# Kernel optimization log

Hardware: AMD Instinct MI355X
Metric: run time of the kernel (lower is better)

Reference implementation:

```python
import jax, jax.numpy as jnp
import numpy as np

LORA_SCALING = 1.0 / 4.0  # lora_alpha / lora_rank
NUM_HEADS = 16
HEAD_DIM = 64
ROPE_BASE = 20000.0


def rotate_half(x):
    x1, x2 = jnp.split(x, 2, axis=-1)
    return jnp.concatenate([-x2, x1], axis=-1)


def setup_inputs() -> dict:
    key = jax.random.key(0)
    ks = jax.random.split(key, 8)
    B, S, D = 8, 1024, 1024
    hidden_states = jax.random.normal(ks[0], (B, S, D), jnp.float32)
    attention_mask = jnp.zeros((B, 1, 1, S), jnp.float32)
    # real rotary tables (HF style: duplicated half-dim freqs)
    inv_freq = 1.0 / (ROPE_BASE ** (jnp.arange(0, HEAD_DIM, 2, dtype=jnp.float32) / HEAD_DIM))
    t = jnp.arange(S, dtype=jnp.float32)
    freqs = jnp.outer(t, inv_freq)                      # [S, hd/2]
    emb = jnp.concatenate([freqs, freqs], axis=-1)      # [S, hd]
    cos = jnp.broadcast_to(jnp.cos(emb)[None], (B, S, HEAD_DIM))
    sin = jnp.broadcast_to(jnp.sin(emb)[None], (B, S, HEAD_DIM))
    adapter_mask = jax.random.randint(ks[1], (B,), 0, 5, jnp.int32)
    Wqkv_weight = jax.random.normal(ks[2], (3 * D, D), jnp.float32) * 0.02
    Wqkv_bias = jax.random.normal(ks[3], (3 * D,), jnp.float32) * 0.02
    lora_A = jax.random.normal(ks[4], (5, 4, D), jnp.float32) * 0.02
    lora_B = jax.random.normal(ks[5], (5, 3 * D, 4), jnp.float32) * 0.02
    return dict(hidden_states=hidden_states, attention_mask=attention_mask,
                cos=cos, sin=sin, adapter_mask=adapter_mask,
                Wqkv_weight=Wqkv_weight, Wqkv_bias=Wqkv_bias,
                lora_A=lora_A, lora_B=lora_B)


def reference(hidden_states, attention_mask, cos, sin, adapter_mask,
              Wqkv_weight, Wqkv_bias, lora_A, lora_B):
    B, S, D = hidden_states.shape
    H, hd = NUM_HEADS, HEAD_DIM
    # fused QKV projection with per-task LoRA (gather adapters per batch row)
    base = jnp.einsum('bsd,od->bso', hidden_states, Wqkv_weight) + Wqkv_bias
    A_t = lora_A[adapter_mask]                    # [B, r, D]
    B_t = lora_B[adapter_mask]                    # [B, 3D, r]
    lo = jnp.einsum('bsd,brd->bsr', hidden_states, A_t)
    delta = jnp.einsum('bsr,bor->bso', lo, B_t) * LORA_SCALING
    qkv = (base + delta).reshape(B, S, 3, H, hd)
    q = qkv[:, :, 0].transpose(0, 2, 1, 3)        # [B,H,S,hd]
    k = qkv[:, :, 1].transpose(0, 2, 1, 3)
    v = qkv[:, :, 2].transpose(0, 2, 1, 3)
    # inline RoPE
    c = cos[:, None, :, :]
    s = sin[:, None, :, :]
    q = q * c + rotate_half(q) * s
    k = k * c + rotate_half(k) * s
    # eager SDPA
    scaling = hd ** -0.5
    scores = jnp.einsum('bhqd,bhkd->bhqk', q, k) * scaling + attention_mask
    attn = jax.nn.softmax(scores, axis=-1)
    out = jnp.einsum('bhqk,bhkd->bhqd', attn, v)
    return out.transpose(0, 2, 1, 3).reshape(B, S, H * hd)
```

## Files before the change

### kernel.cpp

```cpp
#include <hip/hip_runtime.h>
#include <hip/hip_bf16.h>
#include <stdint.h>

typedef __attribute__((ext_vector_type(8))) short short8;
typedef __attribute__((ext_vector_type(4))) float f32x4;
typedef unsigned short ushort_t;

#define MFMA16(a, b, c) __builtin_amdgcn_mfma_f32_16x16x32_bf16((a), (b), (c), 0, 0, 0)
#define EXP2F(x) __builtin_amdgcn_exp2f(x)
#define BAR() __builtin_amdgcn_s_barrier()


__device__ __forceinline__ float bf2f(unsigned short u) {
    union { unsigned int i; float f; } x; x.i = ((unsigned int)u) << 16; return x.f;
}
__device__ __forceinline__ unsigned short f2bf(float f) {
    union { float f; unsigned int i; } x; x.f = f;
    unsigned int i = x.i;
    i = i + 0x7FFFu + ((i >> 16) & 1u);
    return (unsigned short)(i >> 16);
}
__device__ __forceinline__ unsigned int pack2(float a, float b) {
    return (unsigned int)f2bf(a) | ((unsigned int)f2bf(b) << 16);
}
__device__ __forceinline__ void glds16(const void* gsrc, void* ldst) {
    __builtin_amdgcn_global_load_lds(
        (const __attribute__((address_space(1))) unsigned int*)gsrc,
        (__attribute__((address_space(3))) unsigned int*)ldst, 16, 0, 0);
}

__global__ __launch_bounds__(256) void prep_kernel(
    const float* __restrict__ hidden,
    const float* __restrict__ W,
    const float* __restrict__ loraA,
    const int* __restrict__ adapter_mask,
    ushort_t* __restrict__ Hb,
    ushort_t* __restrict__ Wb,
    float4* __restrict__ lo)
{
    int tid = threadIdx.x;
    int wave = tid >> 6, lane = tid & 63;
    int row = blockIdx.x * 4 + wave;
    if (row < 8192) {
        int b = row >> 10;
        int a = adapter_mask[b];
        const float4* hp = (const float4*)(hidden + (size_t)row * 1024);
        float4 hv[4];
#pragma unroll
        for (int c = 0; c < 4; ++c) hv[c] = hp[c * 64 + lane];
#pragma unroll
        for (int c = 0; c < 4; ++c) {
            uint2 pk;
            pk.x = pack2(hv[c].x, hv[c].y);
            pk.y = pack2(hv[c].z, hv[c].w);
            *(uint2*)(Hb + (size_t)row * 1024 + c * 256 + lane * 4) = pk;
        }
        const float4* Ap = (const float4*)(loraA + (size_t)a * 4096);
        float acc[4];
#pragma unroll
        for (int r = 0; r < 4; ++r) {
            float s = 0.f;
#pragma unroll
            for (int c = 0; c < 4; ++c) {
                float4 av = Ap[(size_t)r * 256 + c * 64 + lane];
                s += hv[c].x * av.x + hv[c].y * av.y + hv[c].z * av.z + hv[c].w * av.w;
            }
            acc[r] = s;
        }
        for (int off = 32; off > 0; off >>= 1)
#pragma unroll
            for (int r = 0; r < 4; ++r) acc[r] += __shfl_xor(acc[r], off);
        if (lane == 0) lo[row] = make_float4(acc[0], acc[1], acc[2], acc[3]);
    } else {
        int rw = row - 8192;
        const float4* wp = (const float4*)(W + (size_t)rw * 1024);
        float4 wv[4];
#pragma unroll
        for (int c = 0; c < 4; ++c) wv[c] = wp[c * 64 + lane];
#pragma unroll
        for (int c = 0; c < 4; ++c) {
            uint2 pk;
            pk.x = pack2(wv[c].x, wv[c].y);
            pk.y = pack2(wv[c].z, wv[c].w);
            *(uint2*)(Wb + (size_t)rw * 1024 + c * 256 + lane * 4) = pk;
        }
    }
}

__global__ __launch_bounds__(512, 2) void qkv_gemm_kernel(
    const ushort_t* __restrict__ Hb,
    const ushort_t* __restrict__ Wb,
    const float* __restrict__ bias,
    const float4* __restrict__ lo,
    const float* __restrict__ loraB,
    const int* __restrict__ adapter_mask,
    const float* __restrict__ cosp,
    const float* __restrict__ sinp,
    ushort_t* __restrict__ qw,
    ushort_t* __restrict__ kw,
    ushort_t* __restrict__ vt)
{
    __shared__ __align__(16) ushort_t As[2][16384];
    __shared__ __align__(16) ushort_t Bs[2][16384];
    int tid = threadIdx.x;
    int wave = tid >> 6, lane = tid & 63, quad = lane >> 4, l16 = lane & 15;
    int wm = wave >> 2, wn = wave & 3;

    int wg = (blockIdx.x & 7) * 48 + (blockIdx.x >> 3);
    int bx = wg % 12, by = wg / 12;
    int n0 = bx * 256;
    int m0 = by * 256;

    int r_ = tid >> 3, c_ = (tid & 7) ^ (r_ & 7);
    const ushort_t* pA0 = Hb + (size_t)(m0 +   0 + r_) * 1024 + c_ * 8;
    const ushort_t* pA1 = Hb + (size_t)(m0 +  64 + r_) * 1024 + c_ * 8;
    const ushort_t* pA2 = Hb + (size_t)(m0 + 128 + r_) * 1024 + c_ * 8;
    const ushort_t* pA3 = Hb + (size_t)(m0 + 192 + r_) * 1024 + c_ * 8;
    const ushort_t* pB0 = Wb + (size_t)(n0 +   0 + r_) * 1024 + c_ * 8;
    const ushort_t* pB1 = Wb + (size_t)(n0 +  64 + r_) * 1024 + c_ * 8;
    const ushort_t* pB2 = Wb + (size_t)(n0 + 128 + r_) * 1024 + c_ * 8;
    const ushort_t* pB3 = Wb + (size_t)(n0 + 192 + r_) * 1024 + c_ * 8;
    char* stA0 = (char*)&As[0][0] + wave * 1024;
    char* stB0 = (char*)&Bs[0][0] + wave * 1024;

    f32x4 acc[8][4];
#pragma unroll
    for (int i = 0; i < 8; ++i)
#pragma unroll
        for (int j = 0; j < 4; ++j) acc[i][j] = (f32x4)0.f;

    glds16(pB0, stB0);          glds16(pB1, stB0 + 8192);
    glds16(pB2, stB0 + 16384);  glds16(pB3, stB0 + 24576);
    glds16(pA0, stA0);          glds16(pA1, stA0 + 8192);
    glds16(pA2, stA0 + 16384);  glds16(pA3, stA0 + 24576);
    glds16(pB0 + 64, stB0 + 32768);          glds16(pB1 + 64, stB0 + 32768 + 8192);
    glds16(pB2 + 64, stB0 + 32768 + 16384);  glds16(pB3 + 64, stB0 + 32768 + 24576);

#pragma unroll 2
    for (int t = 0; t < 16; ++t) {
        int cur = t & 1;
        const char* rdA = (const char*)&As[0][0] + cur * 32768;
        const char* rdB = (const char*)&Bs[0][0] + cur * 32768;
        char* sA = stA0 + (cur ^ 1) * 32768;
        char* sB = stB0 + cur * 32768;
        int kA = (t + 1) << 6;
        int kB = (t + 2) << 6;

        if (t < 15) { asm volatile("s_waitcnt vmcnt(4)" ::: "memory"); }
        else        { asm volatile("s_waitcnt vmcnt(0)" ::: "memory"); }
        BAR();
        if (t < 15) {
            glds16(pA0 + kA, sA);          glds16(pA1 + kA, sA + 8192);
            glds16(pA2 + kA, sA + 16384);  glds16(pA3 + kA, sA + 24576);
        }
        short8 bfr[4][2];
#pragma unroll
        for (int ni = 0; ni < 4; ++ni) {
            int rb = ni * 16 + l16;
            bfr[ni][0] = *(const short8*)(rdB + wn * 8192 + (rb * 8 + ((quad    ) ^ (rb & 7))) * 16);
            bfr[ni][1] = *(const short8*)(rdB + wn * 8192 + (rb * 8 + ((quad + 4) ^ (rb & 7))) * 16);
        }
        asm volatile("s_waitcnt lgkmcnt(0)" ::: "memory");
        BAR();
        if (t < 14) {
            glds16(pB0 + kB, sB);          glds16(pB1 + kB, sB + 8192);
            glds16(pB2 + kB, sB + 16384);  glds16(pB3 + kB, sB + 24576);
        }
        __builtin_amdgcn_s_setprio(1);
#pragma unroll
        for (int mi = 0; mi < 8; ++mi) {
            int u = wm * 2 + (mi >> 2);
            int rr = (mi & 3) * 16 + l16;
            short8 a0 = *(const short8*)(rdA + u * 8192 + (rr * 8 + ((quad    ) ^ (rr & 7))) * 16);
            short8 a1 = *(const short8*)(rdA + u * 8192 + (rr * 8 + ((quad + 4) ^ (rr & 7))) * 16);
            acc[mi][0] = MFMA16(a0, bfr[0][0], acc[mi][0]);
            acc[mi][1] = MFMA16(a0, bfr[1][0], acc[mi][1]);
            acc[mi][2] = MFMA16(a0, bfr[2][0], acc[mi][2]);
            acc[mi][3] = MFMA16(a0, bfr[3][0], acc[mi][3]);
            acc[mi][0] = MFMA16(a1, bfr[0][1], acc[mi][0]);
            acc[mi][1] = MFMA16(a1, bfr[1][1], acc[mi][1]);
            acc[mi][2] = MFMA16(a1, bfr[2][1], acc[mi][2]);
            acc[mi][3] = MFMA16(a1, bfr[3][1], acc[mi][3]);
        }
        __builtin_amdgcn_s_setprio(0);
    }

    int t_qkv = n0 >> 10;
    int b = m0 >> 10;
    int a_idx = adapter_mask[b];
    float bi[4], bb[4][4];
    int cpos[4], chh[4];
#pragma unroll
    for (int ni = 0; ni < 4; ++ni) {
        int c = n0 + wn * 64 + ni * 16 + l16;
        bi[ni] = bias[c];
        const float* Bp = loraB + ((size_t)a_idx * 3072 + c) * 4;
        bb[ni][0] = Bp[0]; bb[ni][1] = Bp[1]; bb[ni][2] = Bp[2]; bb[ni][3] = Bp[3];
        cpos[ni] = c & 63; chh[ni] = (c >> 6) & 15;
    }
#pragma unroll
    for (int mi = 0; mi < 8; ++mi) {
        float vals[4][4];
        int mrow0 = m0 + wm * 128 + mi * 16 + quad * 4;
#pragma unroll
        for (int r = 0; r < 4; ++r) {
            float4 lov = lo[mrow0 + r];
#pragma unroll
            for (int ni = 0; ni < 4; ++ni)
                vals[r][ni] = acc[mi][ni][r] + bi[ni]
                      + 0.25f * (lov.x * bb[ni][0] + lov.y * bb[ni][1]
                               + lov.z * bb[ni][2] + lov.w * bb[ni][3]);
        }
        int s0 = mrow0 & 1023;
        if (t_qkv < 2) {
#pragma unroll
            for (int r = 0; r < 4; ++r) {
                int s = s0 + r;
                size_t cb = ((size_t)b * 1024 + s) * 64;
                float cA = cosp[cb + l16],      sA_ = sinp[cb + l16];
                float cB = cosp[cb + 16 + l16], sB_ = sinp[cb + 16 + l16];
                float w0 = vals[r][0] * cA - vals[r][2] * sA_;
                float w2 = vals[r][2] * cA + vals[r][0] * sA_;
                float w1 = vals[r][1] * cB - vals[r][3] * sB_;
                float w3 = vals[r][3] * cB + vals[r][1] * sB_;
                float v[4] = {w0, w1, w2, w3};
#pragma unroll
                for (int ni = 0; ni < 4; ++ni) {
                    size_t bh = (size_t)b * 16 + chh[ni];
                    ushort_t ob = f2bf(v[ni]);
                    if (t_qkv == 0) qw[(bh * 1024 + s) * 64 + cpos[ni]] = ob;
                    else            kw[(bh * 1024 + s) * 64 + cpos[ni]] = ob;
                }
            }
        } else {
#pragma unroll
            for (int ni = 0; ni < 4; ++ni) {
                uint2 pk;
                pk.x = pack2(vals[0][ni], vals[1][ni]);
                pk.y = pack2(vals[2][ni], vals[3][ni]);
                size_t bh = (size_t)b * 16 + chh[ni];
                *(uint2*)&vt[(bh * 64 + cpos[ni]) * 1024 + s0] = pk;
            }
        }
    }
}

__global__ __launch_bounds__(256, 2) void attn_kernel(
    const ushort_t* __restrict__ qw,
    const ushort_t* __restrict__ kw,
    const ushort_t* __restrict__ vt,
    const float* __restrict__ mask,
    float* __restrict__ out)
{
    __shared__ __align__(16) ushort_t Kt[3][4096];
    __shared__ __align__(16) ushort_t Vt[3][4096];
    __shared__ __align__(16) ushort_t Ps[4][32][72];
    __shared__ float mlds[1024];
    const float KSCALE = 0.125f * 1.44269504f;
    int tid = threadIdx.x;
    int wave = tid >> 6, lane = tid & 63, quad = lane >> 4, l16 = lane & 15;
    int id = blockIdx.x;
    int qp = id >> 7;
    int bh = id & 127;
    int b = bh >> 4, h = bh & 15;
    size_t base = (size_t)bh * 65536;
    int q0 = qp * 256 + wave * 32;

    for (int i = tid; i < 1024; i += 256) mlds[i] = mask[b * 1024 + i] * 1.44269504f;

    const ushort_t* kbase = kw + base;
    const ushort_t* vbase = vt + base;

    int n0 = tid, n1 = tid + 256;
    int r0 = n0 >> 3, c0 = (n0 & 7) ^ (r0 & 7);
    int r1 = n1 >> 3, c1 = (n1 & 7) ^ (r1 & 7);

    short8 qf[4][2];
    for (int mt = 0; mt < 4; ++mt) {
        int qr = q0 + (mt >> 1) * 128 + (mt & 1) * 16;
        for (int kt = 0; kt < 2; ++kt)
            qf[mt][kt] = *(const short8*)(qw + base + (size_t)(qr + l16) * 64 + kt * 32 + quad * 8);
    }

    f32x4 oacc[4][4], sum_acc[4];
    for (int mt = 0; mt < 4; ++mt) {
        sum_acc[mt] = (f32x4)0.f;
        for (int nt = 0; nt < 4; ++nt) oacc[mt][nt] = (f32x4)0.f;
    }

    short8 ones;
    for (int j = 0; j < 8; ++j) ones[j] = (short)0x3F80;

    __syncthreads();

    int koff[4][2], voff[4][2];
    for (int nt = 0; nt < 4; ++nt)
        for (int kt = 0; kt < 2; ++kt) {
            int rr = nt * 16 + l16;
            int cc = (kt * 4 + quad) ^ (rr & 7);
            koff[nt][kt] = (rr * 8 + cc) * 8;
            voff[nt][kt] = (rr * 8 + cc) * 8;
        }

    {
        char* kd = (char*)&Kt[0][0] + wave * 1024;
        char* vd = (char*)&Vt[0][0] + wave * 1024;
        glds16(kbase + (size_t)r0 * 64 + c0 * 8, kd);
        glds16(kbase + (size_t)r1 * 64 + c1 * 8, kd + 4096);
        glds16(vbase + (size_t)r0 * 1024 + c0 * 8, vd);
        glds16(vbase + (size_t)r1 * 1024 + c1 * 8, vd + 4096);
        kd = (char*)&Kt[1][0] + wave * 1024;
        vd = (char*)&Vt[1][0] + wave * 1024;
        glds16(kbase + (size_t)(64 + r0) * 64 + c0 * 8, kd);
        glds16(kbase + (size_t)(64 + r1) * 64 + c1 * 8, kd + 4096);
        glds16(vbase + (size_t)r0 * 1024 + 64 + c0 * 8, vd);
        glds16(vbase + (size_t)r1 * 1024 + 64 + c1 * 8, vd + 4096);
    }

    const ushort_t* kR  = &Kt[0][0];  const ushort_t* vR  = &Vt[0][0];
    const ushort_t* kN1 = &Kt[1][0];  const ushort_t* vN1 = &Vt[1][0];
    const ushort_t* kN2 = &Kt[2][0];  const ushort_t* vN2 = &Vt[2][0];

    for (int it = 0; it < 16; ++it) {
        int kt0 = it * 64;
        if (it < 15) { asm volatile("s_waitcnt vmcnt(4)" ::: "memory"); }
        else         { asm volatile("s_waitcnt vmcnt(0)" ::: "memory"); }
        BAR();
        __builtin_amdgcn_sched_barrier(0);
        if (it < 14) {
            int kn = kt0 + 128;
            char* kd = (char*)kN2 + wave * 1024;
            char* vd = (char*)vN2 + wave * 1024;
            glds16(kbase + (size_t)(kn + r0) * 64 + c0 * 8, kd);
            glds16(kbase + (size_t)(kn + r1) * 64 + c1 * 8, kd + 4096);
            glds16(vbase + (size_t)r0 * 1024 + kn + c0 * 8, vd);
            glds16(vbase + (size_t)r1 * 1024 + kn + c1 * 8, vd + 4096);
        }
        float mv[4];
        for (int nt = 0; nt < 4; ++nt) mv[nt] = mlds[kt0 + nt * 16 + l16];

#pragma unroll
        for (int ph = 0; ph < 2; ++ph) {
            f32x4 sacc[2][4];
            {
                short8 kf[4][2];
#pragma unroll
                for (int nt = 0; nt < 4; ++nt)
#pragma unroll
                    for (int kt = 0; kt < 2; ++kt)
                        kf[nt][kt] = *(const short8*)&kR[koff[nt][kt]];
#pragma unroll
                for (int mt = 0; mt < 2; ++mt)
#pragma unroll
                    for (int nt = 0; nt < 4; ++nt) {
                        f32x4 z = (f32x4)0.f;
                        z = MFMA16(qf[ph * 2 + mt][0], kf[nt][0], z);
                        z = MFMA16(qf[ph * 2 + mt][1], kf[nt][1], z);
                        sacc[mt][nt] = z;
                    }
            }
#pragma unroll
            for (int mt = 0; mt < 2; ++mt)
#pragma unroll
                for (int nt = 0; nt < 4; ++nt)
#pragma unroll
                    for (int r = 0; r < 4; ++r) {
                        float p = EXP2F(sacc[mt][nt][r] * KSCALE + mv[nt]);
                        Ps[wave][mt * 16 + quad * 4 + r][nt * 16 + l16] = f2bf(p);
                    }
            short8 pf[2][2];
#pragma unroll
            for (int mt = 0; mt < 2; ++mt)
#pragma unroll
                for (int kt = 0; kt < 2; ++kt)
                    pf[mt][kt] = *(const short8*)&Ps[wave][mt * 16 + l16][kt * 32 + quad * 8];
            {
                short8 vf[4][2];
#pragma unroll
                for (int nt = 0; nt < 4; ++nt)
#pragma unroll
                    for (int kt = 0; kt < 2; ++kt)
                        vf[nt][kt] = *(const short8*)&vR[voff[nt][kt]];
#pragma unroll
                for (int mt = 0; mt < 2; ++mt) {
#pragma unroll
                    for (int nt = 0; nt < 4; ++nt) {
                        oacc[ph * 2 + mt][nt] = MFMA16(pf[mt][0], vf[nt][0], oacc[ph * 2 + mt][nt]);
                        oacc[ph * 2 + mt][nt] = MFMA16(pf[mt][1], vf[nt][1], oacc[ph * 2 + mt][nt]);
                    }
                    sum_acc[ph * 2 + mt] = MFMA16(pf[mt][0], ones, sum_acc[ph * 2 + mt]);
                    sum_acc[ph * 2 + mt] = MFMA16(pf[mt][1], ones, sum_acc[ph * 2 + mt]);
                }
            }
        }
        const ushort_t* tk = kR; kR = kN1; kN1 = kN2; kN2 = tk;
        const ushort_t* tv = vR; vR = vN1; vN1 = vN2; vN2 = tv;
    }

    for (int mt = 0; mt < 4; ++mt) {
        for (int r = 0; r < 4; ++r) {
            float inv = 1.f / sum_acc[mt][r];
            int s = q0 + (mt >> 1) * 128 + (mt & 1) * 16 + quad * 4 + r;
            size_t ob = ((size_t)b * 1024 + s) * 1024 + h * 64;
            for (int nt = 0; nt < 4; ++nt)
                out[ob + nt * 16 + l16] = oacc[mt][nt][r] * inv;
        }
    }
}

extern "C" void kernel_launch(void* const* d_in, const int* in_sizes, int n_in,
                              void* d_out, int out_size, void* d_ws, size_t ws_size,
                              hipStream_t stream)
{
    const float* hidden = (const float*)d_in[0];
    const float* mask   = (const float*)d_in[1];
    const float* cosp   = (const float*)d_in[2];
    const float* sinp   = (const float*)d_in[3];
    const int* adapter_mask = (const int*)d_in[4];
    const float* W      = (const float*)d_in[5];
    const float* bias   = (const float*)d_in[6];
    const float* loraA  = (const float*)d_in[7];
    const float* loraB  = (const float*)d_in[8];
    float* out = (float*)d_out;

    char* ws = (char*)d_ws;
    float4* lo = (float4*)ws;
    ushort_t* qw = (ushort_t*)(ws + (1 << 20));
    ushort_t* kw = qw + (size_t)8 * 16 * 1024 * 64;
    ushort_t* vt = kw + (size_t)8 * 16 * 1024 * 64;

    ushort_t* Hb = (ushort_t*)d_out;
    ushort_t* Wb = Hb + (size_t)8192 * 1024;

    prep_kernel<<<2816, 256, 0, stream>>>(hidden, W, loraA, adapter_mask, Hb, Wb, lo);
    qkv_gemm_kernel<<<384, 512, 0, stream>>>(Hb, Wb, bias, lo, loraB, adapter_mask,
                                             cosp, sinp, qw, kw, vt);
    attn_kernel<<<512, 256, 0, stream>>>(qw, kw, vt, mask, out);
}
```

Before: 236.4 us.

## Shrink QKV GEMM tile to 128x128 with simpler double-buffered K loop

Replaces the 256x256-tile, 512-thread QKV GEMM with a 128x128 tile, 256-thread version that steps K in chunks of 32. It uses a plain double buffer with one __syncthreads per step instead of the staggered A/B prefetch with manual vmcnt waits and priority hints. The grid grows from 384 to 1536 blocks to improve occupancy and CU load balance. In exchange, per-block data reuse drops, global/L2 traffic goes up, and there are more barriers per FLOP.

After: 238.1 us. Within noise of the previous version (+0.8%).

```diff
diff --git a/kernel.cpp b/kernel.cpp
--- a/kernel.cpp
+++ b/kernel.cpp
@@ -87,7 +87,7 @@
     }
 }
 
-__global__ __launch_bounds__(512, 2) void qkv_gemm_kernel(
+__global__ __launch_bounds__(256, 4) void qkv_gemm_kernel(
     const ushort_t* __restrict__ Hb,
     const ushort_t* __restrict__ Wb,
     const float* __restrict__ bias,
@@ -100,89 +100,68 @@
     ushort_t* __restrict__ kw,
     ushort_t* __restrict__ vt)
 {
-    __shared__ __align__(16) ushort_t As[2][16384];
-    __shared__ __align__(16) ushort_t Bs[2][16384];
+    __shared__ __align__(16) ushort_t As[2][4096];
+    __shared__ __align__(16) ushort_t Bs[2][4096];
     int tid = threadIdx.x;
     int wave = tid >> 6, lane = tid & 63, quad = lane >> 4, l16 = lane & 15;
-    int wm = wave >> 2, wn = wave & 3;
-
-    int wg = (blockIdx.x & 7) * 48 + (blockIdx.x >> 3);
-    int bx = wg % 12, by = wg / 12;
-    int n0 = bx * 256;
-    int m0 = by * 256;
-
-    int r_ = tid >> 3, c_ = (tid & 7) ^ (r_ & 7);
-    const ushort_t* pA0 = Hb + (size_t)(m0 +   0 + r_) * 1024 + c_ * 8;
-    const ushort_t* pA1 = Hb + (size_t)(m0 +  64 + r_) * 1024 + c_ * 8;
-    const ushort_t* pA2 = Hb + (size_t)(m0 + 128 + r_) * 1024 + c_ * 8;
-    const ushort_t* pA3 = Hb + (size_t)(m0 + 192 + r_) * 1024 + c_ * 8;
-    const ushort_t* pB0 = Wb + (size_t)(n0 +   0 + r_) * 1024 + c_ * 8;
-    const ushort_t* pB1 = Wb + (size_t)(n0 +  64 + r_) * 1024 + c_ * 8;
-    const ushort_t* pB2 = Wb + (size_t)(n0 + 128 + r_) * 1024 + c_ * 8;
-    const ushort_t* pB3 = Wb + (size_t)(n0 + 192 + r_) * 1024 + c_ * 8;
-    char* stA0 = (char*)&As[0][0] + wave * 1024;
-    char* stB0 = (char*)&Bs[0][0] + wave * 1024;
-
-    f32x4 acc[8][4];
-#pragma unroll
-    for (int i = 0; i < 8; ++i)
+    int mq = (wave >> 1) * 64, nq = (wave & 1) * 64;
+
+    int wg = (blockIdx.x & 7) * 192 + (blockIdx.x >> 3);
+    int bx = wg % 24, by = wg / 24;
+    int n0 = bx * 128;
+    int m0 = by * 128;
+
+    int r_ = tid >> 2;
+    int c_ = (tid & 3) ^ ((tid >> 3) & 3);
+    const ushort_t* pA0 = Hb + (size_t)(m0 + r_) * 1024 + c_ * 8;
+    const ushort_t* pA1 = pA0 + (size_t)64 * 1024;
+    const ushort_t* pB0 = Wb + (size_t)(n0 + r_) * 1024 + c_ * 8;
+    const ushort_t* pB1 = pB0 + (size_t)64 * 1024;
+    char* dA = (char*)&As[0][0] + wave * 1024;
+    char* dB = (char*)&Bs[0][0] + wave * 1024;
+
+    int offA[4], offB[4];
+#pragma unroll
+    for (int i = 0; i < 4; ++i) {
+        int ra = mq + i * 16 + l16;
+        offA[i] = ra * 64 + ((quad ^ ((ra >> 1) & 3)) * 16);
+        int rb = nq + i * 16 + l16;
+        offB[i] = rb * 64 + ((quad ^ ((rb >> 1) & 3)) * 16);
+    }
+
+    f32x4 acc[4][4];
+#pragma unroll
+    for (int i = 0; i < 4; ++i)
 #pragma unroll
         for (int j = 0; j < 4; ++j) acc[i][j] = (f32x4)0.f;
 
-    glds16(pB0, stB0);          glds16(pB1, stB0 + 8192);
-    glds16(pB2, stB0 + 16384);  glds16(pB3, stB0 + 24576);
-    glds16(pA0, stA0);          glds16(pA1, stA0 + 8192);
-    glds16(pA2, stA0 + 16384);  glds16(pA3, stA0 + 24576);
-    glds16(pB0 + 64, stB0 + 32768);          glds16(pB1 + 64, stB0 + 32768 + 8192);
-    glds16(pB2 + 64, stB0 + 32768 + 16384);  glds16(pB3 + 64, stB0 + 32768 + 24576);
+    glds16(pA0, dA);  glds16(pA1, dA + 4096);
+    glds16(pB0, dB);  glds16(pB1, dB + 4096);
+    __syncthreads();
 
 #pragma unroll 2
-    for (int t = 0; t < 16; ++t) {
+    for (int t = 0; t < 32; ++t) {
         int cur = t & 1;
-        const char* rdA = (const char*)&As[0][0] + cur * 32768;
-        const char* rdB = (const char*)&Bs[0][0] + cur * 32768;
-        char* sA = stA0 + (cur ^ 1) * 32768;
-        char* sB = stB0 + cur * 32768;
-        int kA = (t + 1) << 6;
-        int kB = (t + 2) << 6;
-
-        if (t < 15) { asm volatile("s_waitcnt vmcnt(4)" ::: "memory"); }
-        else        { asm volatile("s_waitcnt vmcnt(0)" ::: "memory"); }
-        BAR();
-        if (t < 15) {
-            glds16(pA0 + kA, sA);          glds16(pA1 + kA, sA + 8192);
-            glds16(pA2 + kA, sA + 16384);  glds16(pA3 + kA, sA + 24576);
-        }
-        short8 bfr[4][2];
-#pragma unroll
-        for (int ni = 0; ni < 4; ++ni) {
-            int rb = ni * 16 + l16;
-            bfr[ni][0] = *(const short8*)(rdB + wn * 8192 + (rb * 8 + ((quad    ) ^ (rb & 7))) * 16);
-            bfr[ni][1] = *(const short8*)(rdB + wn * 8192 + (rb * 8 + ((quad + 4) ^ (rb & 7))) * 16);
-        }
-        asm volatile("s_waitcnt lgkmcnt(0)" ::: "memory");
-        BAR();
-        if (t < 14) {
-            glds16(pB0 + kB, sB);          glds16(pB1 + kB, sB + 8192);
-            glds16(pB2 + kB, sB + 16384);  glds16(pB3 + kB, sB + 24576);
-        }
-        __builtin_amdgcn_s_setprio(1);
-#pragma unroll
-        for (int mi = 0; mi < 8; ++mi) {
-            int u = wm * 2 + (mi >> 2);
-            int rr = (mi & 3) * 16 + l16;
-            short8 a0 = *(const short8*)(rdA + u * 8192 + (rr * 8 + ((quad    ) ^ (rr & 7))) * 16);
-            short8 a1 = *(const short8*)(rdA + u * 8192 + (rr * 8 + ((quad + 4) ^ (rr & 7))) * 16);
-            acc[mi][0] = MFMA16(a0, bfr[0][0], acc[mi][0]);
-            acc[mi][1] = MFMA16(a0, bfr[1][0], acc[mi][1]);
-            acc[mi][2] = MFMA16(a0, bfr[2][0], acc[mi][2]);
-            acc[mi][3] = MFMA16(a0, bfr[3][0], acc[mi][3]);
-            acc[mi][0] = MFMA16(a1, bfr[0][1], acc[mi][0]);
-            acc[mi][1] = MFMA16(a1, bfr[1][1], acc[mi][1]);
-            acc[mi][2] = MFMA16(a1, bfr[2][1], acc[mi][2]);
-            acc[mi][3] = MFMA16(a1, bfr[3][1], acc[mi][3]);
-        }
-        __builtin_amdgcn_s_setprio(0);
+        if (t < 31) {
+            int k = (t + 1) * 32;
+            char* sA = dA + (cur ^ 1) * 8192;
+            char* sB = dB + (cur ^ 1) * 8192;
+            glds16(pA0 + k, sA);  glds16(pA1 + k, sA + 4096);
+            glds16(pB0 + k, sB);  glds16(pB1 + k, sB + 4096);
+        }
+        const char* rA = (const char*)&As[0][0] + cur * 8192;
+        const char* rB = (const char*)&Bs[0][0] + cur * 8192;
+        short8 af[4], bf[4];
+#pragma unroll
+        for (int i = 0; i < 4; ++i) af[i] = *(const short8*)(rA + offA[i]);
+#pragma unroll
+        for (int i = 0; i < 4; ++i) bf[i] = *(const short8*)(rB + offB[i]);
+#pragma unroll
+        for (int mi = 0; mi < 4; ++mi)
+#pragma unroll
+            for (int ni = 0; ni < 4; ++ni)
+                acc[mi][ni] = MFMA16(af[mi], bf[ni], acc[mi][ni]);
+        __syncthreads();
     }
 
     int t_qkv = n0 >> 10;
@@ -192,26 +171,26 @@
     int cpos[4], chh[4];
 #pragma unroll
     for (int ni = 0; ni < 4; ++ni) {
-        int c = n0 + wn * 64 + ni * 16 + l16;
+        int c = n0 + nq + ni * 16 + l16;
         bi[ni] = bias[c];
         const float* Bp = loraB + ((size_t)a_idx * 3072 + c) * 4;
         bb[ni][0] = Bp[0]; bb[ni][1] = Bp[1]; bb[ni][2] = Bp[2]; bb[ni][3] = Bp[3];
         cpos[ni] = c & 63; chh[ni] = (c >> 6) & 15;
     }
 #pragma unroll
-    for (int mi = 0; mi < 8; ++mi) {
+    for (int mi = 0; mi < 4; ++mi) {
         float vals[4][4];
-        int mrow0 = m0 + wm * 128 + mi * 16 + quad * 4;
 #pragma unroll
         for (int r = 0; r < 4; ++r) {
-            float4 lov = lo[mrow0 + r];
+            int m = m0 + mq + mi * 16 + quad * 4 + r;
+            float4 lov = lo[m];
 #pragma unroll
             for (int ni = 0; ni < 4; ++ni)
                 vals[r][ni] = acc[mi][ni][r] + bi[ni]
                       + 0.25f * (lov.x * bb[ni][0] + lov.y * bb[ni][1]
                                + lov.z * bb[ni][2] + lov.w * bb[ni][3]);
         }
-        int s0 = mrow0 & 1023;
+        int s0 = (m0 + mq + mi * 16 + quad * 4) & 1023;
         if (t_qkv < 2) {
 #pragma unroll
             for (int r = 0; r < 4; ++r) {
@@ -433,7 +412,7 @@
     ushort_t* Wb = Hb + (size_t)8192 * 1024;
 
     prep_kernel<<<2816, 256, 0, stream>>>(hidden, W, loraA, adapter_mask, Hb, Wb, lo);
-    qkv_gemm_kernel<<<384, 512, 0, stream>>>(Hb, Wb, bias, lo, loraB, adapter_mask,
-                                             cosp, sinp, qw, kw, vt);
+    qkv_gemm_kernel<<<1536, 256, 0, stream>>>(Hb, Wb, bias, lo, loraB, adapter_mask,
+                                              cosp, sinp, qw, kw, vt);
     attn_kernel<<<512, 256, 0, stream>>>(qw, kw, vt, mask, out);
 }
```
